# Kernel tuning notes

Measured on AMD Instinct MI355X. Metric: run time of the kernel, lower is better.

The kernel has to match this reference:

```python
import jax, jax.numpy as jnp
import numpy as np

N_NODES = 100_000
N_EDGES = 1_600_000
D_FEAT = 128
D_HID = 128
D_OUT = 1


def _w(key, fan_in, fan_out):
    # PyG Linear default (glorot-ish); exact init irrelevant for a math reference
    return jax.random.normal(key, (fan_in, fan_out), dtype=jnp.float32) * (1.0 / np.sqrt(fan_in))


def setup_inputs() -> dict:
    key = jax.random.key(0)
    ks = jax.random.split(key, 20)
    inp = {
        "x": jax.random.normal(ks[0], (N_NODES, D_FEAT), dtype=jnp.float32),
        "edge_index": jax.random.randint(ks[1], (2, N_EDGES), 0, N_NODES, dtype=jnp.int32),
    }
    dims = [(D_FEAT, D_HID), (D_HID, D_HID), (D_HID, D_OUT)]
    i = 2
    for li, (din, dout) in enumerate(dims, start=1):
        inp[f"Wk{li}"] = _w(ks[i + 0], din, dout)
        inp[f"Wq{li}"] = _w(ks[i + 1], din, dout)
        inp[f"Wv{li}"] = _w(ks[i + 2], din, dout)
        inp[f"Ws{li}"] = _w(ks[i + 3], din, dout)
        inp[f"b{li}"] = jnp.zeros((dout,), dtype=jnp.float32)
        i += 4
    return inp


def _res_gated_conv(x, src, dst, Wk, Wq, Wv, Ws, b):
    # out_i = Ws x_i + b + sum_{j->i} sigmoid(Wk x_i + Wq x_j) * (Wv x_j)
    k = x @ Wk          # [N, Dout] (keyed by target)
    q = x @ Wq          # [N, Dout] (keyed by source)
    v = x @ Wv          # [N, Dout]
    eta = jax.nn.sigmoid(k[dst] + q[src])          # [E, Dout] edge gate
    msg = eta * v[src]                             # [E, Dout]
    agg = jax.ops.segment_sum(msg, dst, num_segments=x.shape[0])  # scatter-add
    return agg + x @ Ws + b


def reference(x, edge_index, Wk1, Wq1, Wv1, Ws1, b1, Wk2, Wq2, Wv2, Ws2, b2,
              Wk3, Wq3, Wv3, Ws3, b3):
    src = edge_index[0]
    dst = edge_index[1]
    x = jax.nn.relu(_res_gated_conv(x, src, dst, Wk1, Wq1, Wv1, Ws1, b1))
    x = jax.nn.relu(_res_gated_conv(x, src, dst, Wk2, Wq2, Wv2, Ws2, b2))
    return _res_gated_conv(x, src, dst, Wk3, Wq3, Wv3, Ws3, b3)  # [N, 1]
```

## Files before the change

kernel.cpp:

```cpp
#include <hip/hip_runtime.h>
#include <hip/hip_bf16.h>
#include <cstdint>

typedef unsigned short u16;
typedef unsigned int   u32;
typedef __attribute__((ext_vector_type(8))) short bf16x8;
typedef __attribute__((ext_vector_type(4))) float f32x4;

#define NEG_LOG2E -1.44269504088896f

__device__ __forceinline__ float bf2f(u16 u) {
    union { u32 i; float f; } c; c.i = ((u32)u) << 16; return c.f;
}
__device__ __forceinline__ u16 f2bf(float f) {
    union { float f; u32 i; } c; c.f = f;
    u32 x = c.i;
    return (u16)((x + 0x7fffu + ((x >> 16) & 1u)) >> 16);
}
__device__ __forceinline__ void bfu2(u32 p, float& lo, float& hi) {
    union { u32 i; float f; } a, b;
    a.i = p << 16; b.i = p & 0xffff0000u;
    lo = a.f; hi = b.f;
}
__device__ __forceinline__ float gate(float zt) {
    return __builtin_amdgcn_rcpf(1.0f + __builtin_amdgcn_exp2f(zt));
}

#define CSR_CH 2048
#define XS 136

struct P8 { const float* p[8]; };
__global__ __launch_bounds__(256)
void prep_hist_k(P8 wsrc, u16* __restrict__ Wt,
                 const int* __restrict__ dst, int* __restrict__ cnt,
                 int nE, int NA, int nbuck) {
    __shared__ int lh[512];
    int t = threadIdx.x;
    if (blockIdx.x < 64) {
        int mat = blockIdx.x >> 3, seg = blockIdx.x & 7;
        const float* W = wsrc.p[mat];
        u16* T = Wt + (size_t)mat * 16384;
        for (int p = 0; p < 8; ++p) {
            int idx = seg * 2048 + p * 256 + t;
            int k = idx >> 7, n = idx & 127;
            T[n * 128 + k] = f2bf(W[k * 128 + n]);
        }
    } else {
        int b = blockIdx.x - 64;
        for (int i = t; i < nbuck; i += 256) lh[i] = 0;
        __syncthreads();
        int i0 = b * CSR_CH, iend = min(i0 + CSR_CH, nE);
        for (int i = i0 + t; i < iend; i += 256) atomicAdd(&lh[dst[i] >> 8], 1);
        __syncthreads();
        for (int i = t; i < nbuck; i += 256) cnt[i * NA + b] = lh[i];
    }
}

__global__ __launch_bounds__(256)
void scan_part_k(const int* __restrict__ arr, int* __restrict__ part, int M) {
    __shared__ int wsum[4];
    int t = threadIdx.x, lane = t & 63, wave = t >> 6;
    int i0 = blockIdx.x * 1024 + t * 4;
    int s = 0;
    for (int j = 0; j < 4; ++j) { int i = i0 + j; if (i < M) s += arr[i]; }
    for (int off = 32; off > 0; off >>= 1) s += __shfl_xor(s, off);
    if (lane == 0) wsum[wave] = s;
    __syncthreads();
    if (t == 0) part[blockIdx.x] = wsum[0] + wsum[1] + wsum[2] + wsum[3];
}

__global__ __launch_bounds__(256)
void scan_emit2_k(const int* __restrict__ arr, const int* __restrict__ part,
                  int* __restrict__ outp, int M, int total, int nparts) {
    __shared__ int sh[512];
    __shared__ int woff[4];
    int t = threadIdx.x, lane = t & 63, wave = t >> 6;
    sh[t]       = (t < nparts)       ? part[t]       : 0;
    sh[t + 256] = (t + 256 < nparts) ? part[t + 256] : 0;
    __syncthreads();
    for (int off = 1; off < 512; off <<= 1) {
        int u0 = (t >= off)       ? sh[t - off]       : 0;
        int u1 = (t + 256 >= off) ? sh[t + 256 - off] : 0;
        __syncthreads();
        sh[t] += u0; sh[t + 256] += u1;
        __syncthreads();
    }
    int base = (blockIdx.x == 0) ? 0 : sh[blockIdx.x - 1];
    __syncthreads();

    int i0 = blockIdx.x * 1024 + t * 4;
    int d[4]; int s = 0;
    for (int j = 0; j < 4; ++j) { int i = i0 + j; d[j] = (i < M) ? arr[i] : 0; s += d[j]; }
    int ws = s;
    for (int off = 1; off < 64; off <<= 1) {
        int u = __shfl_up(ws, off);
        if (lane >= off) ws += u;
    }
    if (lane == 63) woff[wave] = ws;
    __syncthreads();
    for (int w = 0; w < wave; ++w) base += woff[w];
    int ex = base + ws - s;
    for (int j = 0; j < 4; ++j) {
        int i = i0 + j;
        if (i < M) outp[i] = ex;
        ex += d[j];
    }
    if (blockIdx.x == 0 && t == 0) outp[M] = total;
}

__device__ __forceinline__
void sortB_body(const u32* __restrict__ tkey, const int* __restrict__ scnt,
                int* __restrict__ rowp, int* __restrict__ ssrc,
                int NA, int N, int nE, int b, int* h, int* offv) {
    int t = threadIdx.x;
    int base = scnt[b * NA];
    int endp = scnt[(b + 1) * NA];
    h[t] = 0;
    __syncthreads();
    for (int i = base + t; i < endp; i += 256)
        atomicAdd(&h[tkey[i] >> 24], 1);
    __syncthreads();
    int v = h[t];
    offv[t] = v;
    __syncthreads();
    for (int d = 1; d < 256; d <<= 1) {
        int u = (t >= d) ? offv[t - d] : 0;
        __syncthreads();
        offv[t] += u;
        __syncthreads();
    }
    int ex = offv[t] - v;
    __syncthreads();
    offv[t] = ex;
    h[t] = 0;
    __syncthreads();
    int dglob = b * 256 + t;
    if (dglob < N) rowp[dglob] = base + ex;
    if (b == 0 && t == 0) rowp[N] = nE;
    for (int i = base + t; i < endp; i += 256) {
        u32 k = tkey[i];
        int loc = k >> 24;
        int r = atomicAdd(&h[loc], 1);
        ssrc[base + offv[loc] + r] = (int)(k & 0xFFFFFFu);
    }
}

__global__ __launch_bounds__(256)
void sortB_k(const u32* __restrict__ tkey, const int* __restrict__ scnt,
             int* __restrict__ rowp, int* __restrict__ ssrc,
             int NA, int N, int nE) {
    __shared__ int h[256];
    __shared__ int offv[256];
    sortB_body(tkey, scnt, rowp, ssrc, NA, N, nE, blockIdx.x, h, offv);
}

template<int F32>
__device__ __forceinline__
void gemm_body(int bid, u16* xs,
               const void* __restrict__ Xv, const u16* __restrict__ Wt,
               const float* __restrict__ bias,
               u16* __restrict__ KS, u16* __restrict__ QV, int nrows)
{
    const int tid  = threadIdx.x;
    const int wave = tid >> 6, lane = tid & 63;
    const int quad = lane >> 4, l16 = lane & 15;
    const int r0 = bid * 128;

    for (int p = 0; p < 8; ++p) {
        int c = p * 256 + tid;
        int row = c >> 4;
        int col = (c & 15) * 8;
        int gr = r0 + row; if (gr >= nrows) gr = nrows - 1;
        if (F32) {
            const float* sp = (const float*)Xv + (size_t)gr * 128 + col;
            float4 f0 = *(const float4*)(sp);
            float4 f1 = *(const float4*)(sp + 4);
            uint4 st;
            st.x = ((u32)f2bf(f0.y) << 16) | f2bf(f0.x);
            st.y = ((u32)f2bf(f0.w) << 16) | f2bf(f0.z);
            st.z = ((u32)f2bf(f1.y) << 16) | f2bf(f1.x);
            st.w = ((u32)f2bf(f1.w) << 16) | f2bf(f1.z);
            *(uint4*)(&xs[row * XS + col]) = st;
        } else {
            uint4 d = *(const uint4*)((const u16*)Xv + (size_t)gr * 128 + col);
            *(uint4*)(&xs[row * XS + col]) = d;
        }
    }
    __syncthreads();

    const int cbase = wave * 32;

    for (int pass = 0; pass < 2; ++pass) {
        const u16* WA = Wt + (size_t)(pass ? 0 : 1) * 16384;
        const u16* WB = Wt + (size_t)(pass ? 3 : 2) * 16384;

        bf16x8 afA0[4], afA1[4], afB0[4], afB1[4];
        for (int kt = 0; kt < 4; ++kt) {
            const int ro0 = (cbase + l16)      * 128 + kt * 32 + quad * 8;
            const int ro1 = (cbase + 16 + l16) * 128 + kt * 32 + quad * 8;
            afA0[kt] = *(const bf16x8*)(WA + ro0);
            afA1[kt] = *(const bf16x8*)(WA + ro1);
            afB0[kt] = *(const bf16x8*)(WB + ro0);
            afB1[kt] = *(const bf16x8*)(WB + ro1);
        }

        float4 bias4[2];
        if (pass) {
            bias4[0] = *(const float4*)(bias + cbase + quad * 4);
            bias4[1] = *(const float4*)(bias + cbase + 16 + quad * 4);
        }

        for (int nt = 0; nt < 8; ++nt) {
            f32x4 aA0 = (f32x4)0.0f, aA1 = (f32x4)0.0f;
            f32x4 aB0 = (f32x4)0.0f, aB1 = (f32x4)0.0f;
            for (int kt = 0; kt < 4; ++kt) {
                bf16x8 b = *(const bf16x8*)&xs[(nt * 16 + l16) * XS + kt * 32 + quad * 8];
                aA0 = __builtin_amdgcn_mfma_f32_16x16x32_bf16(afA0[kt], b, aA0, 0, 0, 0);
                aA1 = __builtin_amdgcn_mfma_f32_16x16x32_bf16(afA1[kt], b, aA1, 0, 0, 0);
                aB0 = __builtin_amdgcn_mfma_f32_16x16x32_bf16(afB0[kt], b, aB0, 0, 0, 0);
                aB1 = __builtin_amdgcn_mfma_f32_16x16x32_bf16(afB1[kt], b, aB1, 0, 0, 0);
            }
            int node = r0 + nt * 16 + l16;
            if (node >= nrows) continue;
            u16* rowbase = (pass ? KS : QV) + (size_t)node * 256;
            {
                float x0 = aA0[0] * NEG_LOG2E, x1 = aA0[1] * NEG_LOG2E;
                float x2 = aA0[2] * NEG_LOG2E, x3 = aA0[3] * NEG_LOG2E;
                float y0 = aB0[0], y1 = aB0[1], y2 = aB0[2], y3 = aB0[3];
                if (pass) { y0 += bias4[0].x; y1 += bias4[0].y; y2 += bias4[0].z; y3 += bias4[0].w; }
                uint4 out;
                out.x = ((u32)f2bf(x1) << 16) | f2bf(x0);
                out.y = ((u32)f2bf(x3) << 16) | f2bf(x2);
                out.z = ((u32)f2bf(y1) << 16) | f2bf(y0);
                out.w = ((u32)f2bf(y3) << 16) | f2bf(y2);
                *(uint4*)(rowbase + 2 * (cbase + quad * 4)) = out;
            }
            {
                float x0 = aA1[0] * NEG_LOG2E, x1 = aA1[1] * NEG_LOG2E;
                float x2 = aA1[2] * NEG_LOG2E, x3 = aA1[3] * NEG_LOG2E;
                float y0 = aB1[0], y1 = aB1[1], y2 = aB1[2], y3 = aB1[3];
                if (pass) { y0 += bias4[1].x; y1 += bias4[1].y; y2 += bias4[1].z; y3 += bias4[1].w; }
                uint4 out;
                out.x = ((u32)f2bf(x1) << 16) | f2bf(x0);
                out.y = ((u32)f2bf(x3) << 16) | f2bf(x2);
                out.z = ((u32)f2bf(y1) << 16) | f2bf(y0);
                out.w = ((u32)f2bf(y3) << 16) | f2bf(y2);
                *(uint4*)(rowbase + 2 * (cbase + 16 + quad * 4)) = out;
            }
        }
    }
}

__global__ __launch_bounds__(256, 2)
void sortA_gemm1(const int* __restrict__ src, const int* __restrict__ dst,
                 const int* __restrict__ scnt, u32* __restrict__ tkey,
                 int nE, int NA, int nbuck, int gb,
                 const float* __restrict__ x0, const u16* __restrict__ Wt,
                 const float* __restrict__ bias,
                 u16* __restrict__ KS, u16* __restrict__ QV, int N)
{
    __shared__ u16 xs[128 * XS];
    if ((int)blockIdx.x < gb) {
        gemm_body<1>(blockIdx.x, xs, x0, Wt, bias, KS, QV, N);
    } else {
        int* lh    = (int*)xs;
        int* lbase = lh + 512;
        int t = threadIdx.x, b = blockIdx.x - gb;
        for (int i = t; i < nbuck; i += 256) { lh[i] = 0; lbase[i] = scnt[i * NA + b]; }
        __syncthreads();
        int i0 = b * CSR_CH, iend = min(i0 + CSR_CH, nE);
        for (int i = i0 + t; i < iend; i += 256) {
            int d = dst[i], s = src[i];
            int bk = d >> 8;
            int r = atomicAdd(&lh[bk], 1);
            tkey[lbase[bk] + r] = ((u32)(d & 255) << 24) | (u32)s;
        }
    }
}

__global__ __launch_bounds__(256, 2)
void gemm_l2(const u16* __restrict__ X, const u16* __restrict__ Wt,
             const float* __restrict__ bias,
             u16* __restrict__ KS, u16* __restrict__ QV, int nrows)
{
    __shared__ u16 xs[128 * XS];
    gemm_body<0>(blockIdx.x, xs, X, Wt, bias, KS, QV, nrows);
}

template<int MODE>
__global__ __launch_bounds__(256)
void edge_csr2(const int* __restrict__ rowp, const int* __restrict__ ssrc,
               const u16* __restrict__ KS, const u16* __restrict__ QV,
               u16* __restrict__ Xout,
               const float* __restrict__ Wk3, const float* __restrict__ Wq3,
               const float* __restrict__ Wv3, const float* __restrict__ Ws3,
               const float* __restrict__ b3,
               float* __restrict__ k3, float2* __restrict__ qv3,
               float* __restrict__ s3, int N)
{
    const int lane = threadIdx.x & 63;
    const int half = lane >> 5;
    const int t    = lane & 31;
    int gw = blockIdx.x * (blockDim.x >> 6) + (threadIdx.x >> 6);
    int nw = gridDim.x * (blockDim.x >> 6);

    float4 wk4, wq4, wv4, ws4;
    float bias3 = 0.0f;
    if (MODE == 1) {
        wk4 = *(const float4*)(Wk3 + 4 * t);
        wq4 = *(const float4*)(Wq3 + 4 * t);
        wv4 = *(const float4*)(Wv3 + 4 * t);
        ws4 = *(const float4*)(Ws3 + 4 * t);
        bias3 = b3[0];
    }

#define LOAD2(S0, S1) (*((const uint4*)(QV + (size_t)(half ? (S1) : (S0)) * 256) + t))
#define COMP(QVv, A0, A1, A2, A3)                                             \
    {                                                                         \
        float q0_, q1_, q2_, q3_, v0_, v1_, v2_, v3_;                         \
        bfu2((QVv).x, q0_, q1_); bfu2((QVv).y, q2_, q3_);                     \
        bfu2((QVv).z, v0_, v1_); bfu2((QVv).w, v2_, v3_);                     \
        A0 += gate(k0 + q0_) * v0_;  A1 += gate(k1 + q1_) * v1_;              \
        A2 += gate(k2 + q2_) * v2_;  A3 += gate(k3v + q3_) * v3_;             \
    }
#define LOADG(SVV, G, RA, RB)                                                 \
    {                                                                         \
        int s0_ = __builtin_amdgcn_readlane(SVV, 4 * (G));                    \
        int s1_ = __builtin_amdgcn_readlane(SVV, 4 * (G) + 1);                \
        int s2_ = __builtin_amdgcn_readlane(SVV, 4 * (G) + 2);                \
        int s3_ = __builtin_amdgcn_readlane(SVV, 4 * (G) + 3);                \
        RA = LOAD2(s0_, s1_); RB = LOAD2(s2_, s3_);                           \
    }

    int d = gw;
    int beg = 0, end = 0, sv = 0;
    uint4 ks; ks.x = ks.y = ks.z = ks.w = 0u;
    if (d < N) {
        beg = rowp[d]; end = rowp[d + 1];
        int e  = beg + lane;
        int ec = (end > beg) ? ((e < end) ? e : end - 1) : 0;
        sv = ssrc[ec];
        ks = *((const uint4*)KS + (size_t)d * 32 + t);
    }
    int havePF = 0;
    uint4 pA, pB;
    pA.x = pA.y = pA.z = pA.w = 0u;
    pB = pA;

    while (d < N) {
        int dn = d + nw;
        int begN = 0, endN = 0, svN = 0;
        uint4 ksN; ksN.x = ksN.y = ksN.z = ksN.w = 0u;
        if (dn < N) {
            begN = rowp[dn]; endN = rowp[dn + 1];
            int e  = begN + lane;
            int ec = (endN > begN) ? ((e < endN) ? e : endN - 1) : 0;
            svN = ssrc[ec];
            ksN = *((const uint4*)KS + (size_t)dn * 32 + t);
        }

        float k0, k1, k2, k3v;
        bfu2(ks.x, k0, k1); bfu2(ks.y, k2, k3v);
        float a0 = 0.f, a1 = 0.f, a2 = 0.f, a3 = 0.f;
        float e0 = 0.f, e1 = 0.f, e2 = 0.f, e3 = 0.f;

        for (int base = beg; base < end; base += 64) {
            if (base > beg) {
                int e  = base + lane;
                int ec = (e < end) ? e : end - 1;
                sv = ssrc[ec];
            }
            int m = end - base; if (m > 64) m = 64;
            int ng = m >> 2;
            int j = ng << 2;
            if (ng > 0) {
                uint4 xA, xB, yA, yB;
                if (havePF && base == beg) { xA = pA; xB = pB; }
                else LOADG(sv, 0, xA, xB);
                int g = 1;
                for (; g + 1 < ng; g += 2) {
                    LOADG(sv, g, yA, yB);
                    COMP(xA, a0, a1, a2, a3);
                    COMP(xB, e0, e1, e2, e3);
                    LOADG(sv, g + 1, xA, xB);
                    COMP(yA, a0, a1, a2, a3);
                    COMP(yB, e0, e1, e2, e3);
                }
                if (g < ng) {
                    LOADG(sv, g, yA, yB);
                    COMP(xA, a0, a1, a2, a3);
                    COMP(xB, e0, e1, e2, e3);
                    COMP(yA, a0, a1, a2, a3);
                    COMP(yB, e0, e1, e2, e3);
                } else {
                    COMP(xA, a0, a1, a2, a3);
                    COMP(xB, e0, e1, e2, e3);
                }
            }
            if (j + 2 <= m) {
                int s0 = __builtin_amdgcn_readlane(sv, j);
                int s1 = __builtin_amdgcn_readlane(sv, j + 1);
                uint4 qA = LOAD2(s0, s1);
                COMP(qA, a0, a1, a2, a3);
                j += 2;
            }
            if (j < m) {
                int s0i = __builtin_amdgcn_readlane(sv, j);
                uint4 qv_ = *((const uint4*)(QV + (size_t)s0i * 256) + t);
                float q0_, q1_, q2_, q3_, v0_, v1_, v2_, v3_;
                bfu2(qv_.x, q0_, q1_); bfu2(qv_.y, q2_, q3_);
                bfu2(qv_.z, v0_, v1_); bfu2(qv_.w, v2_, v3_);
                if (half == 0) {
                    a0 += gate(k0 + q0_) * v0_;  a1 += gate(k1 + q1_) * v1_;
                    a2 += gate(k2 + q2_) * v2_;  a3 += gate(k3v + q3_) * v3_;
                }
            }
        }

        havePF = 0;
        if (dn < N) {
            int mN = endN - begN; if (mN > 64) mN = 64;
            if ((mN >> 2) > 0) {
                int s0_ = __builtin_amdgcn_readlane(svN, 0);
                int s1_ = __builtin_amdgcn_readlane(svN, 1);
                int s2_ = __builtin_amdgcn_readlane(svN, 2);
                int s3_ = __builtin_amdgcn_readlane(svN, 3);
                pA = LOAD2(s0_, s1_);
                pB = LOAD2(s2_, s3_);
                havePF = 1;
            }
        }
#undef LOADG
#undef LOAD2
#undef COMP

        a0 += e0; a1 += e1; a2 += e2; a3 += e3;
        a0 += __shfl_xor(a0, 32);
        a1 += __shfl_xor(a1, 32);
        a2 += __shfl_xor(a2, 32);
        a3 += __shfl_xor(a3, 32);

        float s0f, s1f, s2f, s3f;
        bfu2(ks.z, s0f, s1f); bfu2(ks.w, s2f, s3f);
        float r0 = fmaxf(s0f + a0, 0.f);
        float r1 = fmaxf(s1f + a1, 0.f);
        float r2 = fmaxf(s2f + a2, 0.f);
        float r3 = fmaxf(s3f + a3, 0.f);

        if (MODE == 0) {
            if (half == 0) {
                uint2 st;
                st.x = ((u32)f2bf(r1) << 16) | f2bf(r0);
                st.y = ((u32)f2bf(r3) << 16) | f2bf(r2);
                *(uint2*)(Xout + (size_t)d * 128 + t * 4) = st;
            }
        } else {
            float pk = r0 * wk4.x + r1 * wk4.y + r2 * wk4.z + r3 * wk4.w;
            float pq = r0 * wq4.x + r1 * wq4.y + r2 * wq4.z + r3 * wq4.w;
            float pv = r0 * wv4.x + r1 * wv4.y + r2 * wv4.z + r3 * wv4.w;
            float ps = r0 * ws4.x + r1 * ws4.y + r2 * ws4.z + r3 * ws4.w;
            for (int off = 1; off < 32; off <<= 1) {
                pk += __shfl_xor(pk, off);
                pq += __shfl_xor(pq, off);
                pv += __shfl_xor(pv, off);
                ps += __shfl_xor(ps, off);
            }
            if (lane == 0) {
                k3[d]  = NEG_LOG2E * pk;
                qv3[d] = make_float2(NEG_LOG2E * pq, pv);
                s3[d]  = ps + bias3;
            }
        }

        d = dn; beg = begN; end = endN; sv = svN; ks = ksN;
    }
}

__global__ __launch_bounds__(256)
void edge3_csr(const int* __restrict__ rowp, const int* __restrict__ ssrc,
               const float* __restrict__ k3, const float2* __restrict__ qv3,
               const float* __restrict__ s3, float* __restrict__ outp, int N)
{
    int lane = threadIdx.x & 63;
    int gw = blockIdx.x * (blockDim.x >> 6) + (threadIdx.x >> 6);
    int nw = gridDim.x * (blockDim.x >> 6);

    int d = gw;
    int beg = 0, end = 0, sv = 0;
    float kd = 0.f, sd = 0.f;
    if (d < N) {
        beg = rowp[d]; end = rowp[d + 1];
        int e  = beg + lane;
        int ec = (end > beg) ? ((e < end) ? e : end - 1) : 0;
        sv = ssrc[ec];
        kd = k3[d]; sd = s3[d];
    }
    while (d < N) {
        int dn = d + nw;
        int begN = 0, endN = 0, svN = 0;
        float kdN = 0.f, sdN = 0.f;
        if (dn < N) {
            begN = rowp[dn]; endN = rowp[dn + 1];
            int e  = begN + lane;
            int ec = (endN > begN) ? ((e < endN) ? e : endN - 1) : 0;
            svN = ssrc[ec];
            kdN = k3[dn]; sdN = s3[dn];
        }

        float sum = 0.0f;
        int m = end - beg;
        if (lane < m) {
            float2 qv = qv3[sv];
            sum = gate(kd + qv.x) * qv.y;
        }
        for (int e = beg + 64 + lane; e < end; e += 64) {
            float2 qv = qv3[ssrc[e]];
            sum += gate(kd + qv.x) * qv.y;
        }
        for (int off = 32; off > 0; off >>= 1) sum += __shfl_xor(sum, off);
        if (lane == 0) outp[d] = sd + sum;

        d = dn; beg = begN; end = endN; sv = svN; kd = kdN; sd = sdN;
    }
}

extern "C" void kernel_launch(void* const* d_in, const int* in_sizes, int n_in,
                              void* d_out, int out_size, void* d_ws, size_t ws_size,
                              hipStream_t stream)
{
    const float* x0 = (const float*)d_in[0];
    const int*   ei = (const int*)d_in[1];
    const int    N  = in_sizes[0] / 128;
    const int    E  = in_sizes[1] / 2;
    const int* src = ei;
    const int* dst = ei + E;

    const int NBUCK = (N + 255) >> 8;
    const int NA    = (E + CSR_CH - 1) / CSR_CH;
    const int M     = NBUCK * NA;
    const int nparts = (M + 1023) / 1024;

    char* ws = (char*)d_ws;
    size_t off = 0;
    auto carve = [&](size_t bytes) { void* p = ws + off; off += (bytes + 255) & ~(size_t)255; return p; };
    u16*    Wt   = (u16*)carve((size_t)8 * 16384 * sizeof(u16));
    u16*    bufX = (u16*)carve((size_t)N * 128 * sizeof(u16));
    u16*    KS   = (u16*)carve((size_t)N * 256 * sizeof(u16));
    u16*    QV   = (u16*)carve((size_t)N * 256 * sizeof(u16));
    int*    ssrc = (int*)carve((size_t)E * sizeof(int));
    u32*    tkey = (u32*)carve((size_t)E * sizeof(u32));
    int*    rowp = (int*)carve((size_t)(N + 1) * sizeof(int));
    int*    cnt  = (int*)carve((size_t)M * sizeof(int));
    int*    scnt = (int*)carve((size_t)(M + 1) * sizeof(int));
    int*    part = (int*)carve((size_t)512 * sizeof(int));
    float*  k3   = (float*)carve((size_t)N * sizeof(float));
    float2* qv3  = (float2*)carve((size_t)N * sizeof(float2));
    float*  s3   = (float*)carve((size_t)N * sizeof(float));

    P8 wp;
    wp.p[0] = (const float*)d_in[2];  wp.p[1] = (const float*)d_in[3];
    wp.p[2] = (const float*)d_in[4];  wp.p[3] = (const float*)d_in[5];
    wp.p[4] = (const float*)d_in[7];  wp.p[5] = (const float*)d_in[8];
    wp.p[6] = (const float*)d_in[9];  wp.p[7] = (const float*)d_in[10];

    int gb = (N + 127) / 128;

    prep_hist_k<<<64 + NA, 256, 0, stream>>>(wp, Wt, dst, cnt, E, NA, NBUCK);
    scan_part_k<<<nparts, 256, 0, stream>>>(cnt, part, M);
    scan_emit2_k<<<nparts, 256, 0, stream>>>(cnt, part, scnt, M, E, nparts);
    sortA_gemm1<<<gb + NA, 256, 0, stream>>>(src, dst, scnt, tkey, E, NA, NBUCK, gb,
        x0, Wt, (const float*)d_in[6], KS, QV, N);
    sortB_k<<<NBUCK, 256, 0, stream>>>(tkey, scnt, rowp, ssrc, NA, N, E);
    edge_csr2<0><<<4096, 256, 0, stream>>>(rowp, ssrc, KS, QV, bufX,
        nullptr, nullptr, nullptr, nullptr, nullptr, nullptr, nullptr, nullptr, N);
    gemm_l2<<<gb, 256, 0, stream>>>(bufX, Wt + 4 * 16384, (const float*)d_in[11], KS, QV, N);
    edge_csr2<1><<<4096, 256, 0, stream>>>(rowp, ssrc, KS, QV, nullptr,
        (const float*)d_in[12], (const float*)d_in[13], (const float*)d_in[14],
        (const float*)d_in[15], (const float*)d_in[16],
        k3, qv3, s3, N);
    edge3_csr<<<2048, 256, 0, stream>>>(rowp, ssrc, k3, qv3, s3, (float*)d_out, N);
}
```

Before: 495.2 us.

## Fuse layer-1 edge aggregation with layer-2 GEMM through shared memory

Adds a fused kernel in which each 128-row block aggregates its own 128 destination nodes (32 per wave, walked sequentially) and writes the ReLU'd bf16 features into LDS. It then runs the layer-2 GEMM from LDS, writing into separate KS2/QV2 buffers when workspace allows. This drops the bufX global write/read round trip and one launch. The cost is a fixed per-block node partition instead of grid-stride balancing, which may suffer from degree imbalance and lower occupancy (launch bounds 256,2 with LDS).

```diff
diff --git a/kernel.cpp b/kernel.cpp
--- a/kernel.cpp
+++ b/kernel.cpp
@@ -156,16 +156,10 @@
 
 template<int F32>
 __device__ __forceinline__
-void gemm_body(int bid, u16* xs,
-               const void* __restrict__ Xv, const u16* __restrict__ Wt,
-               const float* __restrict__ bias,
-               u16* __restrict__ KS, u16* __restrict__ QV, int nrows)
+void gemm_stage(int bid, u16* xs, const void* __restrict__ Xv, int nrows)
 {
-    const int tid  = threadIdx.x;
-    const int wave = tid >> 6, lane = tid & 63;
-    const int quad = lane >> 4, l16 = lane & 15;
+    const int tid = threadIdx.x;
     const int r0 = bid * 128;
-
     for (int p = 0; p < 8; ++p) {
         int c = p * 256 + tid;
         int row = c >> 4;
@@ -186,8 +180,16 @@
             *(uint4*)(&xs[row * XS + col]) = d;
         }
     }
-    __syncthreads();
-
+}
+
+__device__ __forceinline__
+void gemm_core(int r0, const u16* xs, const u16* __restrict__ Wt,
+               const float* __restrict__ bias,
+               u16* __restrict__ KS, u16* __restrict__ QV, int nrows)
+{
+    const int lane = threadIdx.x & 63;
+    const int wave = threadIdx.x >> 6;
+    const int quad = lane >> 4, l16 = lane & 15;
     const int cbase = wave * 32;
 
     for (int pass = 0; pass < 2; ++pass) {
@@ -261,7 +263,9 @@
 {
     __shared__ u16 xs[128 * XS];
     if ((int)blockIdx.x < gb) {
-        gemm_body<1>(blockIdx.x, xs, x0, Wt, bias, KS, QV, N);
+        gemm_stage<1>(blockIdx.x, xs, x0, N);
+        __syncthreads();
+        gemm_core(blockIdx.x * 128, xs, Wt, bias, KS, QV, N);
     } else {
         int* lh    = (int*)xs;
         int* lbase = lh + 512;
@@ -284,35 +288,10 @@
              u16* __restrict__ KS, u16* __restrict__ QV, int nrows)
 {
     __shared__ u16 xs[128 * XS];
-    gemm_body<0>(blockIdx.x, xs, X, Wt, bias, KS, QV, nrows);
-}
-
-template<int MODE>
-__global__ __launch_bounds__(256)
-void edge_csr2(const int* __restrict__ rowp, const int* __restrict__ ssrc,
-               const u16* __restrict__ KS, const u16* __restrict__ QV,
-               u16* __restrict__ Xout,
-               const float* __restrict__ Wk3, const float* __restrict__ Wq3,
-               const float* __restrict__ Wv3, const float* __restrict__ Ws3,
-               const float* __restrict__ b3,
-               float* __restrict__ k3, float2* __restrict__ qv3,
-               float* __restrict__ s3, int N)
-{
-    const int lane = threadIdx.x & 63;
-    const int half = lane >> 5;
-    const int t    = lane & 31;
-    int gw = blockIdx.x * (blockDim.x >> 6) + (threadIdx.x >> 6);
-    int nw = gridDim.x * (blockDim.x >> 6);
-
-    float4 wk4, wq4, wv4, ws4;
-    float bias3 = 0.0f;
-    if (MODE == 1) {
-        wk4 = *(const float4*)(Wk3 + 4 * t);
-        wq4 = *(const float4*)(Wq3 + 4 * t);
-        wv4 = *(const float4*)(Wv3 + 4 * t);
-        ws4 = *(const float4*)(Ws3 + 4 * t);
-        bias3 = b3[0];
-    }
+    gemm_stage<0>(blockIdx.x, xs, X, nrows);
+    __syncthreads();
+    gemm_core(blockIdx.x * 128, xs, Wt, bias, KS, QV, nrows);
+}
 
 #define LOAD2(S0, S1) (*((const uint4*)(QV + (size_t)(half ? (S1) : (S0)) * 256) + t))
 #define COMP(QVv, A0, A1, A2, A3)                                             \
@@ -332,10 +311,25 @@
         RA = LOAD2(s0_, s1_); RB = LOAD2(s2_, s3_);                           \
     }
 
-    int d = gw;
+__global__ __launch_bounds__(256, 2)
+void edge1_gemm2(const int* __restrict__ rowp, const int* __restrict__ ssrc,
+                 const u16* __restrict__ KS, const u16* __restrict__ QV,
+                 const u16* __restrict__ Wt2, const float* __restrict__ bias2,
+                 u16* __restrict__ KS2, u16* __restrict__ QV2, int N)
+{
+    __shared__ u16 xs[128 * XS];
+    const int lane = threadIdx.x & 63;
+    const int half = lane >> 5;
+    const int t    = lane & 31;
+    const int wave = threadIdx.x >> 6;
+    const int r0b  = blockIdx.x * 128;
+
+    int d    = r0b + wave * 32;
+    int dEnd = min(d + 32, N);
+
     int beg = 0, end = 0, sv = 0;
     uint4 ks; ks.x = ks.y = ks.z = ks.w = 0u;
-    if (d < N) {
+    if (d < dEnd) {
         beg = rowp[d]; end = rowp[d + 1];
         int e  = beg + lane;
         int ec = (end > beg) ? ((e < end) ? e : end - 1) : 0;
@@ -347,11 +341,11 @@
     pA.x = pA.y = pA.z = pA.w = 0u;
     pB = pA;
 
-    while (d < N) {
-        int dn = d + nw;
+    while (d < dEnd) {
+        int dn = d + 1;
         int begN = 0, endN = 0, svN = 0;
         uint4 ksN; ksN.x = ksN.y = ksN.z = ksN.w = 0u;
-        if (dn < N) {
+        if (dn < dEnd) {
             begN = rowp[dn]; endN = rowp[dn + 1];
             int e  = begN + lane;
             int ec = (endN > begN) ? ((e < endN) ? e : endN - 1) : 0;
@@ -418,6 +412,159 @@
         }
 
         havePF = 0;
+        if (dn < dEnd) {
+            int mN = endN - begN; if (mN > 64) mN = 64;
+            if ((mN >> 2) > 0) {
+                int s0_ = __builtin_amdgcn_readlane(svN, 0);
+                int s1_ = __builtin_amdgcn_readlane(svN, 1);
+                int s2_ = __builtin_amdgcn_readlane(svN, 2);
+                int s3_ = __builtin_amdgcn_readlane(svN, 3);
+                pA = LOAD2(s0_, s1_);
+                pB = LOAD2(s2_, s3_);
+                havePF = 1;
+            }
+        }
+
+        a0 += e0; a1 += e1; a2 += e2; a3 += e3;
+        a0 += __shfl_xor(a0, 32);
+        a1 += __shfl_xor(a1, 32);
+        a2 += __shfl_xor(a2, 32);
+        a3 += __shfl_xor(a3, 32);
+
+        float s0f, s1f, s2f, s3f;
+        bfu2(ks.z, s0f, s1f); bfu2(ks.w, s2f, s3f);
+        float r0 = fmaxf(s0f + a0, 0.f);
+        float r1 = fmaxf(s1f + a1, 0.f);
+        float r2 = fmaxf(s2f + a2, 0.f);
+        float r3 = fmaxf(s3f + a3, 0.f);
+
+        if (half == 0) {
+            uint2 st;
+            st.x = ((u32)f2bf(r1) << 16) | f2bf(r0);
+            st.y = ((u32)f2bf(r3) << 16) | f2bf(r2);
+            *(uint2*)(&xs[(d - r0b) * XS + t * 4]) = st;
+        }
+
+        d = dn; beg = begN; end = endN; sv = svN; ks = ksN;
+    }
+
+    __syncthreads();
+    gemm_core(r0b, xs, Wt2, bias2, KS2, QV2, N);
+}
+
+template<int MODE>
+__global__ __launch_bounds__(256)
+void edge_csr2(const int* __restrict__ rowp, const int* __restrict__ ssrc,
+               const u16* __restrict__ KS, const u16* __restrict__ QV,
+               u16* __restrict__ Xout,
+               const float* __restrict__ Wk3, const float* __restrict__ Wq3,
+               const float* __restrict__ Wv3, const float* __restrict__ Ws3,
+               const float* __restrict__ b3,
+               float* __restrict__ k3, float2* __restrict__ qv3,
+               float* __restrict__ s3, int N)
+{
+    const int lane = threadIdx.x & 63;
+    const int half = lane >> 5;
+    const int t    = lane & 31;
+    int gw = blockIdx.x * (blockDim.x >> 6) + (threadIdx.x >> 6);
+    int nw = gridDim.x * (blockDim.x >> 6);
+
+    float4 wk4, wq4, wv4, ws4;
+    float bias3 = 0.0f;
+    if (MODE == 1) {
+        wk4 = *(const float4*)(Wk3 + 4 * t);
+        wq4 = *(const float4*)(Wq3 + 4 * t);
+        wv4 = *(const float4*)(Wv3 + 4 * t);
+        ws4 = *(const float4*)(Ws3 + 4 * t);
+        bias3 = b3[0];
+    }
+
+    int d = gw;
+    int beg = 0, end = 0, sv = 0;
+    uint4 ks; ks.x = ks.y = ks.z = ks.w = 0u;
+    if (d < N) {
+        beg = rowp[d]; end = rowp[d + 1];
+        int e  = beg + lane;
+        int ec = (end > beg) ? ((e < end) ? e : end - 1) : 0;
+        sv = ssrc[ec];
+        ks = *((const uint4*)KS + (size_t)d * 32 + t);
+    }
+    int havePF = 0;
+    uint4 pA, pB;
+    pA.x = pA.y = pA.z = pA.w = 0u;
+    pB = pA;
+
+    while (d < N) {
+        int dn = d + nw;
+        int begN = 0, endN = 0, svN = 0;
+        uint4 ksN; ksN.x = ksN.y = ksN.z = ksN.w = 0u;
+        if (dn < N) {
+            begN = rowp[dn]; endN = rowp[dn + 1];
+            int e  = begN + lane;
+            int ec = (endN > begN) ? ((e < endN) ? e : endN - 1) : 0;
+            svN = ssrc[ec];
+            ksN = *((const uint4*)KS + (size_t)dn * 32 + t);
+        }
+
+        float k0, k1, k2, k3v;
+        bfu2(ks.x, k0, k1); bfu2(ks.y, k2, k3v);
+        float a0 = 0.f, a1 = 0.f, a2 = 0.f, a3 = 0.f;
+        float e0 = 0.f, e1 = 0.f, e2 = 0.f, e3 = 0.f;
+
+        for (int base = beg; base < end; base += 64) {
+            if (base > beg) {
+                int e  = base + lane;
+                int ec = (e < end) ? e : end - 1;
+                sv = ssrc[ec];
+            }
+            int m = end - base; if (m > 64) m = 64;
+            int ng = m >> 2;
+            int j = ng << 2;
+            if (ng > 0) {
+                uint4 xA, xB, yA, yB;
+                if (havePF && base == beg) { xA = pA; xB = pB; }
+                else LOADG(sv, 0, xA, xB);
+                int g = 1;
+                for (; g + 1 < ng; g += 2) {
+                    LOADG(sv, g, yA, yB);
+                    COMP(xA, a0, a1, a2, a3);
+                    COMP(xB, e0, e1, e2, e3);
+                    LOADG(sv, g + 1, xA, xB);
+                    COMP(yA, a0, a1, a2, a3);
+                    COMP(yB, e0, e1, e2, e3);
+                }
+                if (g < ng) {
+                    LOADG(sv, g, yA, yB);
+                    COMP(xA, a0, a1, a2, a3);
+                    COMP(xB, e0, e1, e2, e3);
+                    COMP(yA, a0, a1, a2, a3);
+                    COMP(yB, e0, e1, e2, e3);
+                } else {
+                    COMP(xA, a0, a1, a2, a3);
+                    COMP(xB, e0, e1, e2, e3);
+                }
+            }
+            if (j + 2 <= m) {
+                int s0 = __builtin_amdgcn_readlane(sv, j);
+                int s1 = __builtin_amdgcn_readlane(sv, j + 1);
+                uint4 qA = LOAD2(s0, s1);
+                COMP(qA, a0, a1, a2, a3);
+                j += 2;
+            }
+            if (j < m) {
+                int s0i = __builtin_amdgcn_readlane(sv, j);
+                uint4 qv_ = *((const uint4*)(QV + (size_t)s0i * 256) + t);
+                float q0_, q1_, q2_, q3_, v0_, v1_, v2_, v3_;
+                bfu2(qv_.x, q0_, q1_); bfu2(qv_.y, q2_, q3_);
+                bfu2(qv_.z, v0_, v1_); bfu2(qv_.w, v2_, v3_);
+                if (half == 0) {
+                    a0 += gate(k0 + q0_) * v0_;  a1 += gate(k1 + q1_) * v1_;
+                    a2 += gate(k2 + q2_) * v2_;  a3 += gate(k3v + q3_) * v3_;
+                }
+            }
+        }
+
+        havePF = 0;
         if (dn < N) {
             int mN = endN - begN; if (mN > 64) mN = 64;
             if ((mN >> 2) > 0) {
@@ -430,9 +577,6 @@
                 havePF = 1;
             }
         }
-#undef LOADG
-#undef LOAD2
-#undef COMP
 
         a0 += e0; a1 += e1; a2 += e2; a3 += e3;
         a0 += __shfl_xor(a0, 32);
@@ -475,6 +619,10 @@
         d = dn; beg = begN; end = endN; sv = svN; ks = ksN;
     }
 }
+
+#undef LOADG
+#undef LOAD2
+#undef COMP
 
 __global__ __launch_bounds__(256)
 void edge3_csr(const int* __restrict__ rowp, const int* __restrict__ ssrc,
@@ -557,6 +705,14 @@
     float2* qv3  = (float2*)carve((size_t)N * sizeof(float2));
     float*  s3   = (float*)carve((size_t)N * sizeof(float));
 
+    size_t ksqv2_bytes = 2 * (((size_t)N * 256 * sizeof(u16) + 255) & ~(size_t)255);
+    bool fused = (off + ksqv2_bytes) <= ws_size;
+    u16 *KS2 = nullptr, *QV2 = nullptr;
+    if (fused) {
+        KS2 = (u16*)carve((size_t)N * 256 * sizeof(u16));
+        QV2 = (u16*)carve((size_t)N * 256 * sizeof(u16));
+    }
+
     P8 wp;
     wp.p[0] = (const float*)d_in[2];  wp.p[1] = (const float*)d_in[3];
     wp.p[2] = (const float*)d_in[4];  wp.p[3] = (const float*)d_in[5];
@@ -571,10 +727,19 @@
     sortA_gemm1<<<gb + NA, 256, 0, stream>>>(src, dst, scnt, tkey, E, NA, NBUCK, gb,
         x0, Wt, (const float*)d_in[6], KS, QV, N);
     sortB_k<<<NBUCK, 256, 0, stream>>>(tkey, scnt, rowp, ssrc, NA, N, E);
-    edge_csr2<0><<<4096, 256, 0, stream>>>(rowp, ssrc, KS, QV, bufX,
-        nullptr, nullptr, nullptr, nullptr, nullptr, nullptr, nullptr, nullptr, N);
-    gemm_l2<<<gb, 256, 0, stream>>>(bufX, Wt + 4 * 16384, (const float*)d_in[11], KS, QV, N);
-    edge_csr2<1><<<4096, 256, 0, stream>>>(rowp, ssrc, KS, QV, nullptr,
+
+    const u16* KSL2 = KS;  const u16* QVL2 = QV;
+    if (fused) {
+        edge1_gemm2<<<gb, 256, 0, stream>>>(rowp, ssrc, KS, QV,
+            Wt + 4 * 16384, (const float*)d_in[11], KS2, QV2, N);
+        KSL2 = KS2; QVL2 = QV2;
+    } else {
+        edge_csr2<0><<<4096, 256, 0, stream>>>(rowp, ssrc, KS, QV, bufX,
+            nullptr, nullptr, nullptr, nullptr, nullptr, nullptr, nullptr, nullptr, N);
+        gemm_l2<<<gb, 256, 0, stream>>>(bufX, Wt + 4 * 16384,
+            (const float*)d_in[11], KS, QV, N);
+    }
+    edge_csr2<1><<<4096, 256, 0, stream>>>(rowp, ssrc, KSL2, QVL2, nullptr,
         (const float*)d_in[12], (const float*)d_in[13], (const float*)d_in[14],
         (const float*)d_in[15], (const float*)d_in[16],
         k3, qv3, s3, N);
```

After: 542.4 us. 1.1x slower.
